# Kernel optimization log

Hardware: AMD Instinct MI355X
Metric: run time of the kernel (lower is better)

## Reference

```python
import jax, jax.numpy as jnp
import numpy as np

HEADS = 4
DIM_HEAD = 32
DIM = 128
HIDDEN = HEADS * DIM_HEAD  # 128
LN_EPS = 1e-6


def setup_inputs() -> dict:
    key = jax.random.key(0)
    ks = jax.random.split(key, 4)
    b, X, Y, Z = 4, 32, 32, 32
    x = jax.random.normal(ks[0], (b, X, Y, Z, DIM), dtype=jnp.float32)
    # 1x1x1 convs are pointwise linears: kernel [in, out]
    w_qkv = jax.random.normal(ks[1], (DIM, 3 * HIDDEN), dtype=jnp.float32) * (DIM ** -0.5)
    w_out = jax.random.normal(ks[2], (HIDDEN, DIM), dtype=jnp.float32) * (HIDDEN ** -0.5)
    b_out = jax.random.normal(ks[3], (DIM,), dtype=jnp.float32) * 0.02
    ln_scale = jnp.ones((DIM,), dtype=jnp.float32)
    ln_bias = jnp.zeros((DIM,), dtype=jnp.float32)
    return {"x": x, "w_qkv": w_qkv, "w_out": w_out, "b_out": b_out,
            "ln_scale": ln_scale, "ln_bias": ln_bias}


def reference(x, w_qkv, w_out, b_out, ln_scale, ln_bias):
    b, X, Y, Z, c = x.shape
    n = X * Y * Z
    scale = DIM_HEAD ** (-0.5)

    # 1x1x1 conv (no bias) == pointwise matmul over channels
    qkv = jnp.einsum('bxyzc,cd->bxyzd', x, w_qkv)  # [b,X,Y,Z,3*hidden]
    q, k, v = jnp.split(qkv, 3, axis=-1)

    # rearrange 'b x y z (h c) -> b h c n'
    def to_bhcn(t):
        return t.reshape(b, n, HEADS, DIM_HEAD).transpose(0, 2, 3, 1)

    q, k, v = to_bhcn(q), to_bhcn(k), to_bhcn(v)

    q = jax.nn.softmax(q, axis=-2) * scale   # softmax over feature dim d
    k = jax.nn.softmax(k, axis=-1)           # softmax over token dim n

    context = jnp.einsum('bhdn,bhcn->bhdc', k, v)   # [b,h,d,c] small d=c=32
    out = jnp.einsum('bhde,bhdn->bhen', context, q) # [b,h,e,n]

    # rearrange 'b h c n -> b x y z (h c)' (cubic volume, matching original)
    out = out.transpose(0, 3, 1, 2).reshape(b, X, Y, Z, HIDDEN)

    # final 1x1x1 conv with bias
    out = jnp.einsum('bxyzh,hc->bxyzc', out, w_out) + b_out

    # LayerNorm over last axis (flax default eps=1e-6, with scale+bias)
    mu = jnp.mean(out, axis=-1, keepdims=True)
    var = jnp.mean(jnp.square(out - mu), axis=-1, keepdims=True)
    out = (out - mu) * jax.lax.rsqrt(var + LN_EPS) * ln_scale + ln_bias
    return out
```

## Files before the change

kernel.cpp:

```cpp
#include <hip/hip_runtime.h>
#include <hip/hip_bf16.h>

typedef _Float16 f16;
typedef _Float16 f16x4 __attribute__((ext_vector_type(4)));
typedef _Float16 f16x8 __attribute__((ext_vector_type(8)));
typedef float f32x4 __attribute__((ext_vector_type(4)));

#define MFMA(a, b, c) __builtin_amdgcn_mfma_f32_16x16x32_f16((a), (b), (c), 0, 0, 0)

#define BB 4
#define NPOS 32768
#define HH 4
#define NBLK 1024
#define NBLK3 2048
#define STATB 2304
#define LDP 136

__device__ __forceinline__ f16x8 ldx8(const float* p) {
  float4 a = *(const float4*)p;
  float4 b = *(const float4*)(p + 4);
  return (f16x8){(f16)a.x, (f16)a.y, (f16)a.z, (f16)a.w,
                 (f16)b.x, (f16)b.y, (f16)b.z, (f16)b.w};
}

__global__ __launch_bounds__(256)
void la_k0_prep(const float* __restrict__ wqkv, const float* __restrict__ wout,
                f16* __restrict__ wkvF, f16* __restrict__ wqF,
                f16* __restrict__ woutT) {
  const int g0 = blockIdx.x * 256 + threadIdx.x;
  for (int i = g0; i < 32768; i += 16384) {
    int j = i & 7, l = (i >> 3) & 63, ks = (i >> 9) & 3, nt = (i >> 11) & 3,
        h = i >> 13;
    int n = 16 * nt + (l & 15);
    int c = 32 * ks + 8 * (l >> 4) + j;
    int col = (n < 32) ? (128 + h * 32 + n) : (256 + h * 32 + (n - 32));
    wkvF[i] = (f16)wqkv[c * 384 + col];
  }
  {
    int i = g0;
    int j = i & 7, l = (i >> 3) & 63, ks = (i >> 9) & 3, a = (i >> 11) & 1,
        h = i >> 12;
    int row = l & 15;
    int n = 8 * (row >> 2) + 4 * a + (row & 3);
    int c = 32 * ks + 8 * (l >> 4) + j;
    wqF[i] = (f16)wqkv[c * 384 + h * 32 + n];
  }
  if (g0 < 128 * 128) {
    int k = g0 & 127, n = g0 >> 7;
    woutT[g0] = (f16)wout[k * 128 + n];
  }
}

__global__ __launch_bounds__(256, 4)
void la_k1_stats(const float* __restrict__ x, const f16* __restrict__ wkvF,
                 char* __restrict__ stats) {
  const int blk = blockIdx.x, t = threadIdx.x;
  const int w = t >> 6, l = t & 63, lg = l >> 4, ln = l & 15;

  __shared__ __align__(16) f16 EV[2][64 * LDP];

  const float* xb = x + (size_t)blk * (128 * 128);
  f16x8 xf[2][4];
#pragma unroll
  for (int mi = 0; mi < 2; ++mi)
#pragma unroll
    for (int ks = 0; ks < 4; ++ks)
      xf[mi][ks] = ldx8(xb + (32 * w + 16 * mi + ln) * 128 + 32 * ks + 8 * lg);

  const f32x4 Z4 = {0.f, 0.f, 0.f, 0.f};

  auto logits = [&](int h, f32x4 (&acc)[2][4]) {
#pragma unroll
    for (int mi = 0; mi < 2; ++mi)
#pragma unroll
      for (int nt = 0; nt < 4; ++nt) acc[mi][nt] = Z4;
#pragma unroll
    for (int ks = 0; ks < 4; ++ks) {
#pragma unroll
      for (int nt = 0; nt < 4; ++nt) {
        f16x8 bf = *(const f16x8*)(wkvF + (((h * 4 + nt) * 4 + ks) << 9) + l * 8);
        acc[0][nt] = MFMA(xf[0][ks], bf, acc[0][nt]);
        acc[1][nt] = MFMA(xf[1][ks], bf, acc[1][nt]);
      }
    }
  };

  auto phaseA = [&](int h, f32x4 (&acc)[2][4]) {
    f16* E = (f16*)EV[h & 1];
    float sl[2] = {0.f, 0.f};
#pragma unroll
    for (int nt = 0; nt < 2; ++nt)
#pragma unroll
      for (int mi = 0; mi < 2; ++mi) {
        float e0 = __expf(acc[mi][nt][0]);
        float e1 = __expf(acc[mi][nt][1]);
        float e2 = __expf(acc[mi][nt][2]);
        float e3 = __expf(acc[mi][nt][3]);
        sl[nt] += (e0 + e1) + (e2 + e3);
        *(f16x4*)&E[(16 * nt + ln) * LDP + 32 * w + 16 * mi + 4 * lg] =
            (f16x4){(f16)e0, (f16)e1, (f16)e2, (f16)e3};
        f32x4 vv = acc[mi][nt + 2];
        *(f16x4*)&E[(32 + 16 * nt + ln) * LDP + 32 * w + 16 * mi + 4 * lg] =
            (f16x4){(f16)vv[0], (f16)vv[1], (f16)vv[2], (f16)vv[3]};
      }
#pragma unroll
    for (int nt = 0; nt < 2; ++nt) {
      sl[nt] += __shfl_xor(sl[nt], 16);
      sl[nt] += __shfl_xor(sl[nt], 32);
    }
    f16* sp = (f16*)(stats + (size_t)(blk * HH + h) * STATB + 2048);
    if (lg == 0) {
      sp[ln * 4 + w] = (f16)sl[0];
      sp[(16 + ln) * 4 + w] = (f16)sl[1];
    }
  };

  auto phaseB = [&](int h) {
    __syncthreads();
    const f16* E = (const f16*)EV[h & 1];
    const int tm = w >> 1, tn = w & 1;
    f32x4 tacc = Z4;
#pragma unroll
    for (int ks = 0; ks < 4; ++ks) {
      f16x8 ea = *(const f16x8*)&E[(16 * tm + ln) * LDP + 32 * ks + 8 * lg];
      f16x8 vb = *(const f16x8*)&E[(32 + 16 * tn + ln) * LDP + 32 * ks + 8 * lg];
      tacc = MFMA(ea, vb, tacc);
    }
    f16* tp = (f16*)(stats + (size_t)(blk * HH + h) * STATB);
#pragma unroll
    for (int r = 0; r < 4; ++r)
      tp[(16 * tm + 4 * lg + r) * 32 + 16 * tn + ln] = (f16)tacc[r];
  };

  f32x4 accA[2][4], accB[2][4];
  logits(0, accA);
  phaseA(0, accA); logits(1, accB); phaseB(0);
  phaseA(1, accB); logits(2, accA); phaseB(1);
  phaseA(2, accA); logits(3, accB); phaseB(2);
  phaseA(3, accB); phaseB(3);
}

__global__ __launch_bounds__(256)
void la_k2_combine(const char* __restrict__ stats, f16* __restrict__ ctxN) {
  const int gid = blockIdx.x;
  const int bh = gid >> 5, d = gid & 31;
  const int b = bh >> 2, h = bh & 3;
  const int t = threadIdx.x, w = t >> 6, l = t & 63;
  const int c = t & 31, grp = t >> 5;
  __shared__ float redt[4][32];
  __shared__ float reds[4];

  float sg = 0.f, tc = 0.f;
  for (int i = grp; i < 256; i += 8) {
    const char* ub = stats + (size_t)((b * 256 + i) * HH + h) * STATB;
    tc += (float)((const f16*)ub)[d * 32 + c];
    f16x4 s4 = *(const f16x4*)(ub + 2048 + d * 8);
    sg += ((float)s4[0] + (float)s4[1]) + ((float)s4[2] + (float)s4[3]);
  }
  tc += __shfl_xor(tc, 32);
  sg += __shfl_xor(sg, 32);
  if (l < 32) redt[w][l] = tc;
  if (l == 0) reds[w] = sg;
  __syncthreads();
  if (t < 32) {
    float tt = (redt[0][t] + redt[1][t]) + (redt[2][t] + redt[3][t]);
    float ss = (reds[0] + reds[1]) + (reds[2] + reds[3]);
    ctxN[((size_t)bh * 32 + d) * 32 + t] = (f16)(tt / ss);
  }
}

__global__ __launch_bounds__(256)
void la_k2b_fold(const f16* __restrict__ ctxN, const f16* __restrict__ woutT,
                 f16* __restrict__ GTF) {
  const int b = blockIdx.x, t = threadIdx.x;
  const int h = t >> 6, l = t & 63, lg = l >> 4, ln = l & 15;
  const f32x4 Z4 = {0.f, 0.f, 0.f, 0.f};

  const f16* cb = ctxN + (size_t)((b * HH + h) * 32) * 32;
  f16x8 bfrag[2];
#pragma unroll
  for (int nt = 0; nt < 2; ++nt)
    bfrag[nt] = *(const f16x8*)(cb + (16 * nt + ln) * 32 + 8 * lg);

  f16* gf = GTF + (size_t)b * 16384;
#pragma unroll
  for (int mt = 0; mt < 8; ++mt) {
    f16x8 af = *(const f16x8*)(woutT + (16 * mt + ln) * 128 + 32 * h + 8 * lg);
#pragma unroll
    for (int nt = 0; nt < 2; ++nt) {
      f32x4 acc = MFMA(af, bfrag[nt], Z4);
#pragma unroll
      for (int r = 0; r < 4; ++r) {
        int dsub = 16 * nt + ln;
        gf[((h * 8 + mt) << 9) + (16 * (dsub >> 3) + 4 * lg + r) * 8 + (dsub & 7)] =
            (f16)acc[r];
      }
    }
  }
}

__global__ __launch_bounds__(256, 5)
void la_k3_out(const float* __restrict__ x, const f16* __restrict__ wqF,
               const f16* __restrict__ GTF, const float* __restrict__ bout,
               const float* __restrict__ lns, const float* __restrict__ lnb,
               float* __restrict__ out) {
  const int blk = blockIdx.x, t = threadIdx.x;
  const int w = t >> 6, l = t & 63, lg = l >> 4, ln = l & 15;
  const int b = blk >> 9;
  const int p0 = blk * 64 + 16 * w;

  const float* xb = x + (size_t)p0 * 128;
  f16x8 xf[4];
#pragma unroll
  for (int ks = 0; ks < 4; ++ks)
    xf[ks] = ldx8(xb + ln * 128 + 32 * ks + 8 * lg);

  const f32x4 Z4 = {0.f, 0.f, 0.f, 0.f};
  const f16* gf = GTF + (size_t)b * 16384;

  f32x4 y[8];
#pragma unroll
  for (int nc = 0; nc < 8; ++nc) y[nc] = Z4;

  auto qlog = [&](int h, f32x4 (&qa)[2]) {
    qa[0] = Z4;
    qa[1] = Z4;
#pragma unroll
    for (int ks = 0; ks < 4; ++ks) {
      f16x8 a0 = *(const f16x8*)(wqF + (((h * 2 + 0) * 4 + ks) << 9) + l * 8);
      f16x8 a1 = *(const f16x8*)(wqF + (((h * 2 + 1) * 4 + ks) << 9) + l * 8);
      qa[0] = MFMA(a0, xf[ks], qa[0]);
      qa[1] = MFMA(a1, xf[ks], qa[1]);
    }
  };

  auto consume = [&](f32x4 (&qa)[2], f16x8& af) {
    float s = 0.f;
#pragma unroll
    for (int mt = 0; mt < 2; ++mt)
#pragma unroll
      for (int r = 0; r < 4; ++r) {
        qa[mt][r] = __expf(qa[mt][r]);
        s += qa[mt][r];
      }
    s += __shfl_xor(s, 16);
    s += __shfl_xor(s, 32);
    const float inv = 0.17677669529663688f / s;
    af = (f16x8){(f16)(qa[0][0] * inv), (f16)(qa[0][1] * inv),
                 (f16)(qa[0][2] * inv), (f16)(qa[0][3] * inv),
                 (f16)(qa[1][0] * inv), (f16)(qa[1][1] * inv),
                 (f16)(qa[1][2] * inv), (f16)(qa[1][3] * inv)};
  };

  auto ymfma = [&](int h, f16x8& af) {
#pragma unroll
    for (int nc = 0; nc < 8; ++nc) {
      f16x8 gfr = *(const f16x8*)(gf + (((h * 8 + nc) << 9) + l * 8));
      y[nc] = MFMA(gfr, af, y[nc]);
    }
  };

  f32x4 qaA[2], qaB[2];
  f16x8 afA, afB;
  qlog(0, qaA); qlog(1, qaB);
  consume(qaA, afA); ymfma(0, afA); qlog(2, qaA);
  consume(qaB, afB); ymfma(1, afB); qlog(3, qaB);
  consume(qaA, afA); ymfma(2, afA);
  consume(qaB, afB); ymfma(3, afB);

#pragma unroll
  for (int nc = 0; nc < 8; ++nc) {
    f32x4 bb = *(const f32x4*)(bout + 16 * nc + 4 * lg);
    y[nc] += bb;
  }

  float s = 0.f;
#pragma unroll
  for (int nc = 0; nc < 8; ++nc)
    s += (y[nc][0] + y[nc][1]) + (y[nc][2] + y[nc][3]);
  s += __shfl_xor(s, 16);
  s += __shfl_xor(s, 32);
  const float mean = s * (1.f / 128.f);
  float v = 0.f;
#pragma unroll
  for (int nc = 0; nc < 8; ++nc)
#pragma unroll
    for (int r = 0; r < 4; ++r) {
      float dv = y[nc][r] - mean;
      v = fmaf(dv, dv, v);
    }
  v += __shfl_xor(v, 16);
  v += __shfl_xor(v, 32);
  const float inv = rsqrtf(v * (1.f / 128.f) + 1e-6f);

  float* op = out + (size_t)(p0 + ln) * 128;
#pragma unroll
  for (int nc = 0; nc < 8; ++nc) {
    f32x4 sv = *(const f32x4*)(lns + 16 * nc + 4 * lg);
    f32x4 b2 = *(const f32x4*)(lnb + 16 * nc + 4 * lg);
    f32x4 o4;
#pragma unroll
    for (int r = 0; r < 4; ++r)
      o4[r] = (y[nc][r] - mean) * inv * sv[r] + b2[r];
    *(f32x4*)(op + 16 * nc + 4 * lg) = o4;
  }
}

extern "C" void kernel_launch(void* const* d_in, const int* in_sizes, int n_in,
                              void* d_out, int out_size, void* d_ws, size_t ws_size,
                              hipStream_t stream) {
  const float* x = (const float*)d_in[0];
  const float* w_qkv = (const float*)d_in[1];
  const float* w_out = (const float*)d_in[2];
  const float* b_out = (const float*)d_in[3];
  const float* ln_s = (const float*)d_in[4];
  const float* ln_b = (const float*)d_in[5];
  float* out = (float*)d_out;

  char* ws = (char*)d_ws;
  char* stats = ws;
  f16* wkvF = (f16*)(ws + 9437184);
  f16* wqF = (f16*)(ws + 9437184 + 65536);
  f16* woutT = (f16*)(ws + 9437184 + 65536 + 32768);
  f16* ctxN = (f16*)(ws + 9437184 + 65536 + 32768 + 32768);
  f16* GTF = (f16*)ws;

  la_k0_prep<<<dim3(64), 256, 0, stream>>>(w_qkv, w_out, wkvF, wqF, woutT);
  la_k1_stats<<<dim3(NBLK), 256, 0, stream>>>(x, wkvF, stats);
  la_k2_combine<<<dim3(512), 256, 0, stream>>>(stats, ctxN);
  la_k2b_fold<<<dim3(BB), 256, 0, stream>>>(ctxN, woutT, GTF);
  la_k3_out<<<dim3(NBLK3), 256, 0, stream>>>(x, wqF, GTF, b_out, ln_s, ln_b, out);
}
```

Before: 87.39 us.

## Fuse stats combine with Wout fold and prefetch GTF fragments in output kernel

Merges the combine and fold kernels into one 16-block kernel. It reduces the per-block stats with vectorized loads, normalizes the context in shared memory, and reads w_out directly, which removes woutT prep, the ctxN round trip and one launch. The output kernel now double-buffers the GTF fragments in registers ahead of the MFMAs, and launch bounds drop to 2 waves to allow the extra registers. The risks are that 16 blocks serialize a 9MB stats reduction on only a few CUs, and that lower occupancy may hurt latency hiding in the output kernel.

```diff
diff --git a/kernel.cpp b/kernel.cpp
--- a/kernel.cpp
+++ b/kernel.cpp
@@ -24,9 +24,8 @@
 }
 
 __global__ __launch_bounds__(256)
-void la_k0_prep(const float* __restrict__ wqkv, const float* __restrict__ wout,
-                f16* __restrict__ wkvF, f16* __restrict__ wqF,
-                f16* __restrict__ woutT) {
+void la_k0_prep(const float* __restrict__ wqkv, f16* __restrict__ wkvF,
+                f16* __restrict__ wqF) {
   const int g0 = blockIdx.x * 256 + threadIdx.x;
   for (int i = g0; i < 32768; i += 16384) {
     int j = i & 7, l = (i >> 3) & 63, ks = (i >> 9) & 3, nt = (i >> 11) & 3,
@@ -44,10 +43,6 @@
     int n = 8 * (row >> 2) + 4 * a + (row & 3);
     int c = 32 * ks + 8 * (l >> 4) + j;
     wqF[i] = (f16)wqkv[c * 384 + h * 32 + n];
-  }
-  if (g0 < 128 * 128) {
-    int k = g0 & 127, n = g0 >> 7;
-    woutT[g0] = (f16)wout[k * 128 + n];
   }
 }
 
@@ -141,54 +136,62 @@
 }
 
 __global__ __launch_bounds__(256)
-void la_k2_combine(const char* __restrict__ stats, f16* __restrict__ ctxN) {
-  const int gid = blockIdx.x;
-  const int bh = gid >> 5, d = gid & 31;
-  const int b = bh >> 2, h = bh & 3;
-  const int t = threadIdx.x, w = t >> 6, l = t & 63;
-  const int c = t & 31, grp = t >> 5;
-  __shared__ float redt[4][32];
-  __shared__ float reds[4];
-
-  float sg = 0.f, tc = 0.f;
-  for (int i = grp; i < 256; i += 8) {
-    const char* ub = stats + (size_t)((b * 256 + i) * HH + h) * STATB;
-    tc += (float)((const f16*)ub)[d * 32 + c];
-    f16x4 s4 = *(const f16x4*)(ub + 2048 + d * 8);
-    sg += ((float)s4[0] + (float)s4[1]) + ((float)s4[2] + (float)s4[3]);
-  }
-  tc += __shfl_xor(tc, 32);
-  sg += __shfl_xor(sg, 32);
-  if (l < 32) redt[w][l] = tc;
-  if (l == 0) reds[w] = sg;
+void la_k2_fold(const char* __restrict__ stats, const float* __restrict__ wout,
+                f16* __restrict__ GTF) {
+  const int bh = blockIdx.x, b = bh >> 2, h = bh & 3;
+  const int t = threadIdx.x, w = t >> 6, l = t & 63, lg = l >> 4, ln = l & 15;
+  const f32x4 Z4 = {0.f, 0.f, 0.f, 0.f};
+
+  __shared__ float tred[256][8];
+  __shared__ float sred[128];
+  __shared__ float ss[32];
+  __shared__ __align__(16) f16 cn[1024];
+
+  {
+    const int sl = t & 127, hf = t >> 7;
+    float a[8] = {0.f, 0.f, 0.f, 0.f, 0.f, 0.f, 0.f, 0.f};
+    for (int i = hf; i < 256; i += 2) {
+      const f16x8 v = *(const f16x8*)(stats +
+          (size_t)((b * 256 + i) * HH + h) * STATB + sl * 16);
+#pragma unroll
+      for (int j = 0; j < 8; ++j) a[j] += (float)v[j];
+    }
+#pragma unroll
+    for (int j = 0; j < 8; ++j) tred[t][j] = a[j];
+  }
+  if (t < 128) {
+    float sa = 0.f;
+    for (int i = 0; i < 256; ++i)
+      sa += (float)*(const f16*)(stats +
+          (size_t)((b * 256 + i) * HH + h) * STATB + 2048 + t * 2);
+    sred[t] = sa;
+  }
   __syncthreads();
-  if (t < 32) {
-    float tt = (redt[0][t] + redt[1][t]) + (redt[2][t] + redt[3][t]);
-    float ss = (reds[0] + reds[1]) + (reds[2] + reds[3]);
-    ctxN[((size_t)bh * 32 + d) * 32 + t] = (f16)(tt / ss);
-  }
-}
-
-__global__ __launch_bounds__(256)
-void la_k2b_fold(const f16* __restrict__ ctxN, const f16* __restrict__ woutT,
-                 f16* __restrict__ GTF) {
-  const int b = blockIdx.x, t = threadIdx.x;
-  const int h = t >> 6, l = t & 63, lg = l >> 4, ln = l & 15;
-  const f32x4 Z4 = {0.f, 0.f, 0.f, 0.f};
-
-  const f16* cb = ctxN + (size_t)((b * HH + h) * 32) * 32;
-  f16x8 bfrag[2];
-#pragma unroll
-  for (int nt = 0; nt < 2; ++nt)
-    bfrag[nt] = *(const f16x8*)(cb + (16 * nt + ln) * 32 + 8 * lg);
+  if (t < 32)
+    ss[t] = (sred[4 * t] + sred[4 * t + 1]) + (sred[4 * t + 2] + sred[4 * t + 3]);
+  __syncthreads();
+  if (t < 128) {
+    const float inv = 1.f / ss[t >> 2];
+    f16x8 c8;
+#pragma unroll
+    for (int j = 0; j < 8; ++j)
+      c8[j] = (f16)((tred[t][j] + tred[t + 128][j]) * inv);
+    *(f16x8*)&cn[t * 8] = c8;
+  }
+  __syncthreads();
 
   f16* gf = GTF + (size_t)b * 16384;
 #pragma unroll
-  for (int mt = 0; mt < 8; ++mt) {
-    f16x8 af = *(const f16x8*)(woutT + (16 * mt + ln) * 128 + 32 * h + 8 * lg);
+  for (int mi = 0; mi < 2; ++mi) {
+    const int mt = 2 * w + mi;
+    f16x8 af;
+#pragma unroll
+    for (int j = 0; j < 8; ++j)
+      af[j] = (f16)wout[(32 * h + 8 * lg + j) * 128 + 16 * mt + ln];
 #pragma unroll
     for (int nt = 0; nt < 2; ++nt) {
-      f32x4 acc = MFMA(af, bfrag[nt], Z4);
+      f16x8 bf = *(const f16x8*)&cn[(16 * nt + ln) * 32 + 8 * lg];
+      f32x4 acc = MFMA(af, bf, Z4);
 #pragma unroll
       for (int r = 0; r < 4; ++r) {
         int dsub = 16 * nt + ln;
@@ -199,7 +202,7 @@
   }
 }
 
-__global__ __launch_bounds__(256, 5)
+__global__ __launch_bounds__(256, 2)
 void la_k3_out(const float* __restrict__ x, const f16* __restrict__ wqF,
                const f16* __restrict__ GTF, const float* __restrict__ bout,
                const float* __restrict__ lns, const float* __restrict__ lnb,
@@ -217,6 +220,11 @@
 
   const f32x4 Z4 = {0.f, 0.f, 0.f, 0.f};
   const f16* gf = GTF + (size_t)b * 16384;
+
+  f16x8 gA[8], gB[8];
+#pragma unroll
+  for (int nc = 0; nc < 8; ++nc)
+    gA[nc] = *(const f16x8*)(gf + ((0 * 8 + nc) << 9) + l * 8);
 
   f32x4 y[8];
 #pragma unroll
@@ -252,21 +260,25 @@
                  (f16)(qa[1][2] * inv), (f16)(qa[1][3] * inv)};
   };
 
-  auto ymfma = [&](int h, f16x8& af) {
-#pragma unroll
-    for (int nc = 0; nc < 8; ++nc) {
-      f16x8 gfr = *(const f16x8*)(gf + (((h * 8 + nc) << 9) + l * 8));
-      y[nc] = MFMA(gfr, af, y[nc]);
-    }
+  auto prefetch = [&](int h, f16x8 (&g)[8]) {
+#pragma unroll
+    for (int nc = 0; nc < 8; ++nc)
+      g[nc] = *(const f16x8*)(gf + (((h * 8 + nc) << 9) + l * 8));
+  };
+
+  auto ymfma = [&](f16x8 (&g)[8], f16x8& af) {
+#pragma unroll
+    for (int nc = 0; nc < 8; ++nc) y[nc] = MFMA(g[nc], af, y[nc]);
   };
 
   f32x4 qaA[2], qaB[2];
   f16x8 afA, afB;
   qlog(0, qaA); qlog(1, qaB);
-  consume(qaA, afA); ymfma(0, afA); qlog(2, qaA);
-  consume(qaB, afB); ymfma(1, afB); qlog(3, qaB);
-  consume(qaA, afA); ymfma(2, afA);
-  consume(qaB, afB); ymfma(3, afB);
+  consume(qaA, afA);
+  prefetch(1, gB); ymfma(gA, afA); qlog(2, qaA); consume(qaB, afB);
+  prefetch(2, gA); ymfma(gB, afB); qlog(3, qaB); consume(qaA, afA);
+  prefetch(3, gB); ymfma(gA, afA); consume(qaB, afB);
+  ymfma(gB, afB);
 
 #pragma unroll
   for (int nc = 0; nc < 8; ++nc) {
@@ -321,13 +333,10 @@
   char* stats = ws;
   f16* wkvF = (f16*)(ws + 9437184);
   f16* wqF = (f16*)(ws + 9437184 + 65536);
-  f16* woutT = (f16*)(ws + 9437184 + 65536 + 32768);
-  f16* ctxN = (f16*)(ws + 9437184 + 65536 + 32768 + 32768);
-  f16* GTF = (f16*)ws;
-
-  la_k0_prep<<<dim3(64), 256, 0, stream>>>(w_qkv, w_out, wkvF, wqF, woutT);
+  f16* GTF = (f16*)(ws + 9437184 + 65536 + 32768);
+
+  la_k0_prep<<<dim3(64), 256, 0, stream>>>(w_qkv, wkvF, wqF);
   la_k1_stats<<<dim3(NBLK), 256, 0, stream>>>(x, wkvF, stats);
-  la_k2_combine<<<dim3(512), 256, 0, stream>>>(stats, ctxN);
-  la_k2b_fold<<<dim3(BB), 256, 0, stream>>>(ctxN, woutT, GTF);
+  la_k2_fold<<<dim3(16), 256, 0, stream>>>(stats, w_out, GTF);
   la_k3_out<<<dim3(NBLK3), 256, 0, stream>>>(x, wqF, GTF, b_out, ln_s, ln_b, out);
 }
```

Measured after the change: 135.3 us. 1.55x slower.
